# Kernel tuning notes

Measured on AMD Instinct MI355X. Metric: run time of the kernel, lower is better.

Reference implementation:

```python
import jax, jax.numpy as jnp
import numpy as np

B = 8192      # sessions
L = 64        # tokens per session
T = B * L     # total tokens
H = 128       # hidden_size
MAX_LEN = 64  # position_emb has MAX_LEN+1 rows


def setup_inputs() -> dict:
    key = jax.random.key(0)
    ks = jax.random.split(key, 10)
    s1 = 1.0 / np.sqrt(H)
    s2 = 1.0 / np.sqrt(2 * H)
    hidden = jax.random.normal(ks[0], (T, H), jnp.float32)
    seq_len = jnp.full((B,), L, dtype=jnp.int32)
    # reversed positions 1..L within each session (<= MAX_LEN)
    reverse_pos = jnp.tile(jnp.arange(L, 0, -1, dtype=jnp.int32), B)
    return {
        "hidden": hidden,
        "pos_table": jax.random.normal(ks[1], (MAX_LEN + 1, H), jnp.float32) * 0.02,
        "W_pos_w": jax.random.normal(ks[2], (H, 2 * H), jnp.float32) * s2,
        "W_pos_b": jax.random.normal(ks[3], (H,), jnp.float32) * s2,
        "W1_w": jax.random.normal(ks[4], (H, H), jnp.float32) * s1,
        "W1_b": jax.random.normal(ks[5], (H,), jnp.float32) * s1,
        "W2_w": jax.random.normal(ks[6], (H, H), jnp.float32) * s1,
        "W2_b": jax.random.normal(ks[7], (H,), jnp.float32) * s1,
        "q_w": jax.random.normal(ks[8], (1, H), jnp.float32) * s1,
        "q_b": jax.random.normal(ks[9], (1,), jnp.float32) * s1,
        "seq_len": seq_len,
        "reverse_pos": reverse_pos,
    }


def reference(hidden, pos_table, W_pos_w, W_pos_b, W1_w, W1_b, W2_w, W2_b,
              q_w, q_b, seq_len, reverse_pos):
    Bn = seq_len.shape[0]
    Tn = hidden.shape[0]
    # token -> session id (replaces the python split loop)
    seg = jnp.repeat(jnp.arange(Bn), seq_len, total_repeat_length=Tn)  # [T]
    # per-session mean, broadcast back to tokens (v_mean_repeat_concat)
    mean = jax.ops.segment_sum(hidden, seg, num_segments=Bn) \
        / seq_len[:, None].astype(hidden.dtype)                        # [B,H]
    mean_rep = mean[seg]                                               # [T,H]
    pos_emb = pos_table[reverse_pos]                                   # [T,H]
    pos_hidden = jnp.tanh(
        jnp.concatenate([hidden, pos_emb], axis=-1) @ W_pos_w.T + W_pos_b
    )                                                                  # [T,H]
    gate = jax.nn.sigmoid(mean_rep @ W1_w.T + W1_b + pos_hidden @ W2_w.T + W2_b)
    alpha = gate @ q_w.T + q_b                                         # [T,1]
    # per-session sum of alpha-weighted tokens (h_s)
    return jax.ops.segment_sum(alpha * hidden, seg, num_segments=Bn)   # [B,H]
```

## Files before the change

kernel.cpp:

```cpp
#include <hip/hip_runtime.h>
#include <hip/hip_bf16.h>

typedef unsigned short u16;
typedef __bf16 bf16x8 __attribute__((ext_vector_type(8)));
typedef float  f32x4  __attribute__((ext_vector_type(4)));

__device__ __forceinline__ unsigned pk2(float a, float b) {
    __hip_bfloat162 h = __float22bfloat162_rn(make_float2(a, b));
    unsigned u; __builtin_memcpy(&u, &h, 4);
    return u;
}
__device__ __forceinline__ u16 f2b1(float f) { return (u16)(pk2(f, f) & 0xFFFFu); }

#define MFMA __builtin_amdgcn_mfma_f32_16x16x32_bf16

__global__ __launch_bounds__(128) void prep_kernel(
    const float* __restrict__ pos_table, const float* __restrict__ Wpw,
    const float* __restrict__ Wpb, const float* __restrict__ W2,
    float* __restrict__ ppK, u16* __restrict__ wb1, u16* __restrict__ wb2)
{
    const int b = blockIdx.x, t = threadIdx.x;
    if (b < 65) {
        const float4* pr = (const float4*)(pos_table + b * 128);
        const float4* wr = (const float4*)(Wpw + t * 256 + 128);
        float acc = Wpb[t];
        #pragma unroll
        for (int k = 0; k < 32; ++k) {
            const float4 p = pr[k], wv = wr[k];
            acc += p.x * wv.x + p.y * wv.y + p.z * wv.z + p.w * wv.w;
        }
        ppK[b * 128 + t] = acc * 2.885390081777927f;
    } else {
        const int j = b - 65;
        const int off = (((j >> 4) * 4 + (t >> 5)) * 16 + (j & 15)) * 32 + (t & 31);
        wb1[off] = f2b1(Wpw[j * 256 + t]);
        wb2[off] = f2b1(W2[j * 128 + t]);
    }
}

__global__ __launch_bounds__(256, 4) void fused_kernel(
    const float* __restrict__ hidden, const int* __restrict__ rpos,
    const float* __restrict__ W1, const float* __restrict__ W1b,
    const float* __restrict__ W2b, const float* __restrict__ qw,
    const float* __restrict__ qb, const float* __restrict__ ppK,
    const u16* __restrict__ wb1g, const u16* __restrict__ wb2g,
    float* __restrict__ out)
{
    __shared__ __align__(16) u16 hbf[128 * 136];
    __shared__ float meanv[256];
    __shared__ float g1s[256];
    __shared__ float qws[128];
    __shared__ float alphas[128];
    __shared__ int   rps[128];

    const int tid = threadIdx.x;
    const int blk = blockIdx.x;
    const int w = tid >> 6;
    const int l = tid & 63;
    const int c = l & 15;
    const int g = l >> 4;
    const int R = 32 * w;
    const float* hsrc = hidden + (size_t)blk * (128 * 128);

    meanv[tid] = 0.f;
    if (tid < 128) { rps[tid] = rpos[blk * 128 + tid]; qws[tid] = qw[tid]; }
    __syncthreads();

    {
        float4 ms0 = {0.f, 0.f, 0.f, 0.f}, ms1 = {0.f, 0.f, 0.f, 0.f};
        #pragma unroll
        for (int i = 0; i < 16; ++i) {
            const int i4 = tid + i * 256;
            const float4 v = ((const float4*)hsrc)[i4];
            const int e = i4 * 4, row = e >> 7, col = e & 127;
            uint2 st; st.x = pk2(v.x, v.y); st.y = pk2(v.z, v.w);
            *(uint2*)&hbf[row * 136 + col] = st;
            if (i < 8) { ms0.x += v.x; ms0.y += v.y; ms0.z += v.z; ms0.w += v.w; }
            else       { ms1.x += v.x; ms1.y += v.y; ms1.z += v.z; ms1.w += v.w; }
        }
        ms0.x += __shfl_xor(ms0.x, 32, 64); ms0.y += __shfl_xor(ms0.y, 32, 64);
        ms0.z += __shfl_xor(ms0.z, 32, 64); ms0.w += __shfl_xor(ms0.w, 32, 64);
        ms1.x += __shfl_xor(ms1.x, 32, 64); ms1.y += __shfl_xor(ms1.y, 32, 64);
        ms1.z += __shfl_xor(ms1.z, 32, 64); ms1.w += __shfl_xor(ms1.w, 32, 64);
        if ((l & 32) == 0) {
            const int mc = (tid * 4) & 127;
            atomicAdd(&meanv[mc],           ms0.x); atomicAdd(&meanv[mc + 1],       ms0.y);
            atomicAdd(&meanv[mc + 2],       ms0.z); atomicAdd(&meanv[mc + 3],       ms0.w);
            atomicAdd(&meanv[128 + mc],     ms1.x); atomicAdd(&meanv[128 + mc + 1], ms1.y);
            atomicAdd(&meanv[128 + mc + 2], ms1.z); atomicAdd(&meanv[128 + mc + 3], ms1.w);
        }
    }
    __syncthreads();

    {
        const int col = tid & 127, s = tid >> 7;
        const float4* wr = (const float4*)(W1 + col * 128);
        const float4* mv = (const float4*)(meanv + s * 128);
        float acc = 0.f;
        #pragma unroll 8
        for (int k4 = 0; k4 < 32; ++k4) {
            const float4 wv = wr[k4], m4 = mv[k4];
            acc += m4.x * wv.x + m4.y * wv.y + m4.z * wv.z + m4.w * wv.w;
        }
        g1s[tid] = W1b[col] + W2b[col] + acc * (1.f / 64.f);
    }

    bf16x8 af[2][4];
    #pragma unroll
    for (int m = 0; m < 2; ++m)
        #pragma unroll
        for (int kk = 0; kk < 4; ++kk)
            af[m][kk] = *(const bf16x8*)&hbf[(R + 16 * m + c) * 136 + kk * 32 + g * 8];

    int pko[2][4];
    #pragma unroll
    for (int m = 0; m < 2; ++m)
        #pragma unroll
        for (int r = 0; r < 4; ++r)
            pko[m][r] = rps[R + 16 * m + 4 * g + r] * 128 + c;

    {
        const u16* wb1p = wb1g + c * 32 + g * 8;
        const float K2 = 2.885390081777927f;
        #pragma unroll
        for (int n = 0; n < 8; ++n) {
            f32x4 acc[2] = {};
            #pragma unroll
            for (int kk = 0; kk < 4; ++kk) {
                const bf16x8 bfr = *(const bf16x8*)(wb1p + n * 2048 + kk * 512);
                acc[0] = MFMA(af[0][kk], bfr, acc[0], 0, 0, 0);
                acc[1] = MFMA(af[1][kk], bfr, acc[1], 0, 0, 0);
            }
            #pragma unroll
            for (int m = 0; m < 2; ++m)
                #pragma unroll
                for (int r = 0; r < 4; ++r) {
                    const float arg = fmaf(acc[m][r], K2, ppK[pko[m][r] + 16 * n]);
                    const float e2 = __builtin_amdgcn_exp2f(arg);
                    const float rc = __builtin_amdgcn_rcpf(e2 + 1.f);
                    hbf[(R + 16 * m + 4 * g + r) * 136 + 16 * n + c] =
                        f2b1(fmaf(-2.f, rc, 1.f));
                }
        }
    }

    bf16x8 af2[2][4];
    #pragma unroll
    for (int m = 0; m < 2; ++m)
        #pragma unroll
        for (int kk = 0; kk < 4; ++kk)
            af2[m][kk] = *(const bf16x8*)&hbf[(R + 16 * m + c) * 136 + kk * 32 + g * 8];

    __syncthreads();

    {
        const u16* wb2p = wb2g + c * 32 + g * 8;
        const float K1 = 1.4426950408889634f;
        const int sw = w >> 1;
        float prt[2][4] = {};
        #pragma unroll
        for (int n = 0; n < 8; ++n) {
            f32x4 acc[2] = {};
            #pragma unroll
            for (int kk = 0; kk < 4; ++kk) {
                const bf16x8 bfr = *(const bf16x8*)(wb2p + n * 2048 + kk * 512);
                acc[0] = MFMA(af2[0][kk], bfr, acc[0], 0, 0, 0);
                acc[1] = MFMA(af2[1][kk], bfr, acc[1], 0, 0, 0);
            }
            const float gv = -K1 * g1s[sw * 128 + 16 * n + c];
            const float qv = qws[16 * n + c];
            #pragma unroll
            for (int m = 0; m < 2; ++m)
                #pragma unroll
                for (int r = 0; r < 4; ++r) {
                    const float arg = fmaf(acc[m][r], -K1, gv);
                    const float e2 = __builtin_amdgcn_exp2f(arg);
                    const float rc = __builtin_amdgcn_rcpf(e2 + 1.f);
                    prt[m][r] = fmaf(rc, qv, prt[m][r]);
                }
        }
        #pragma unroll
        for (int msk = 1; msk <= 8; msk <<= 1)
            #pragma unroll
            for (int m = 0; m < 2; ++m)
                #pragma unroll
                for (int r = 0; r < 4; ++r)
                    prt[m][r] += __shfl_xor(prt[m][r], msk, 64);
        if (c == 0) {
            const float qbv = qb[0];
            #pragma unroll
            for (int m = 0; m < 2; ++m)
                #pragma unroll
                for (int r = 0; r < 4; ++r)
                    alphas[R + 16 * m + 4 * g + r] = prt[m][r] + qbv;
        }
    }
    __syncthreads();

    {
        const int h = tid & 127, p = tid >> 7;
        const float* hs = hsrc + p * (64 * 128) + h;
        float accf = 0.f;
        #pragma unroll 8
        for (int t = 0; t < 64; ++t)
            accf = fmaf(alphas[64 * p + t], hs[t * 128], accf);
        out[(size_t)blk * 256 + tid] = accf;
    }
}

extern "C" void kernel_launch(void* const* d_in, const int* in_sizes, int n_in,
                              void* d_out, int out_size, void* d_ws, size_t ws_size,
                              hipStream_t stream)
{
    const float* hidden    = (const float*)d_in[0];
    const float* pos_table = (const float*)d_in[1];
    const float* Wpw       = (const float*)d_in[2];
    const float* Wpb       = (const float*)d_in[3];
    const float* W1w       = (const float*)d_in[4];
    const float* W1b       = (const float*)d_in[5];
    const float* W2w       = (const float*)d_in[6];
    const float* W2b       = (const float*)d_in[7];
    const float* qw        = (const float*)d_in[8];
    const float* qb        = (const float*)d_in[9];
    const int*   rpos      = (const int*)d_in[11];
    float* out = (float*)d_out;

    const int B = in_sizes[10];

    char* wsb = (char*)d_ws;
    float* ppK = (float*)wsb;
    u16* wb1   = (u16*)(wsb + 33280);
    u16* wb2   = (u16*)(wsb + 33280 + 32768);

    prep_kernel<<<193, 128, 0, stream>>>(pos_table, Wpw, Wpb, W2w,
                                         ppK, wb1, wb2);
    fused_kernel<<<B / 2, 256, 0, stream>>>(hidden, rpos, W1w, W1b, W2b, qw, qb,
                                            ppK, wb1, wb2, out);
}
```

Measured before the change: 481.4 us.

## Assign one session per wavefront and fold mean projection into MFMA

Restructures the fused kernel so each wavefront owns a whole 64-token session. The wavefront loads hidden straight from global into MFMA A-fragments and takes the session mean with shuffles instead of LDS atomics. The W1·mean product now runs as a bf16 MFMA seeded into the gate accumulator, using a W1 copy prepacked in the prep kernel, and the combined bias is precomputed there too. Most block-level barriers go away, but each wave now holds more registers (launch bounds drop to 2 waves/SIMD), and the mean projection loses some precision by moving to bf16.

```diff
diff --git a/kernel.cpp b/kernel.cpp
--- a/kernel.cpp
+++ b/kernel.cpp
@@ -12,12 +12,23 @@
 }
 __device__ __forceinline__ u16 f2b1(float f) { return (u16)(pk2(f, f) & 0xFFFFu); }
 
+__device__ __forceinline__ bf16x8 pack8(const float4 a, const float4 b) {
+    unsigned u0 = pk2(a.x, a.y), u1 = pk2(a.z, a.w);
+    unsigned u2 = pk2(b.x, b.y), u3 = pk2(b.z, b.w);
+    unsigned arr[4] = {u0, u1, u2, u3};
+    bf16x8 r; __builtin_memcpy(&r, arr, 16);
+    return r;
+}
+
 #define MFMA __builtin_amdgcn_mfma_f32_16x16x32_bf16
 
 __global__ __launch_bounds__(128) void prep_kernel(
     const float* __restrict__ pos_table, const float* __restrict__ Wpw,
     const float* __restrict__ Wpb, const float* __restrict__ W2,
-    float* __restrict__ ppK, u16* __restrict__ wb1, u16* __restrict__ wb2)
+    const float* __restrict__ W1, const float* __restrict__ W1b,
+    const float* __restrict__ W2b,
+    float* __restrict__ ppK, u16* __restrict__ wb1, u16* __restrict__ wb2,
+    u16* __restrict__ wb3, float* __restrict__ bsum)
 {
     const int b = blockIdx.x, t = threadIdx.x;
     if (b < 65) {
@@ -35,176 +46,188 @@
         const int off = (((j >> 4) * 4 + (t >> 5)) * 16 + (j & 15)) * 32 + (t & 31);
         wb1[off] = f2b1(Wpw[j * 256 + t]);
         wb2[off] = f2b1(W2[j * 128 + t]);
-    }
-}
-
-__global__ __launch_bounds__(256, 4) void fused_kernel(
+        wb3[off] = f2b1(W1[j * 128 + t]);
+        if (j == 0) bsum[t] = W1b[t] + W2b[t];
+    }
+}
+
+__global__ __launch_bounds__(256, 2) void fused_kernel(
     const float* __restrict__ hidden, const int* __restrict__ rpos,
-    const float* __restrict__ W1, const float* __restrict__ W1b,
-    const float* __restrict__ W2b, const float* __restrict__ qw,
-    const float* __restrict__ qb, const float* __restrict__ ppK,
-    const u16* __restrict__ wb1g, const u16* __restrict__ wb2g,
-    float* __restrict__ out)
+    const float* __restrict__ qw, const float* __restrict__ qb,
+    const float* __restrict__ ppK, const u16* __restrict__ wb1g,
+    const u16* __restrict__ wb2g, const u16* __restrict__ wb3g,
+    const float* __restrict__ bsum, float* __restrict__ out)
 {
-    __shared__ __align__(16) u16 hbf[128 * 136];
-    __shared__ float meanv[256];
-    __shared__ float g1s[256];
-    __shared__ float qws[128];
-    __shared__ float alphas[128];
-    __shared__ int   rps[128];
+    __shared__ __align__(16) u16 phs[4 * 64 * 136];
+    __shared__ __align__(16) float alphas[4 * 64];
 
     const int tid = threadIdx.x;
-    const int blk = blockIdx.x;
     const int w = tid >> 6;
     const int l = tid & 63;
     const int c = l & 15;
     const int g = l >> 4;
-    const int R = 32 * w;
-    const float* hsrc = hidden + (size_t)blk * (128 * 128);
-
-    meanv[tid] = 0.f;
-    if (tid < 128) { rps[tid] = rpos[blk * 128 + tid]; qws[tid] = qw[tid]; }
-    __syncthreads();
-
-    {
-        float4 ms0 = {0.f, 0.f, 0.f, 0.f}, ms1 = {0.f, 0.f, 0.f, 0.f};
-        #pragma unroll
-        for (int i = 0; i < 16; ++i) {
-            const int i4 = tid + i * 256;
-            const float4 v = ((const float4*)hsrc)[i4];
-            const int e = i4 * 4, row = e >> 7, col = e & 127;
-            uint2 st; st.x = pk2(v.x, v.y); st.y = pk2(v.z, v.w);
-            *(uint2*)&hbf[row * 136 + col] = st;
-            if (i < 8) { ms0.x += v.x; ms0.y += v.y; ms0.z += v.z; ms0.w += v.w; }
-            else       { ms1.x += v.x; ms1.y += v.y; ms1.z += v.z; ms1.w += v.w; }
-        }
-        ms0.x += __shfl_xor(ms0.x, 32, 64); ms0.y += __shfl_xor(ms0.y, 32, 64);
-        ms0.z += __shfl_xor(ms0.z, 32, 64); ms0.w += __shfl_xor(ms0.w, 32, 64);
-        ms1.x += __shfl_xor(ms1.x, 32, 64); ms1.y += __shfl_xor(ms1.y, 32, 64);
-        ms1.z += __shfl_xor(ms1.z, 32, 64); ms1.w += __shfl_xor(ms1.w, 32, 64);
-        if ((l & 32) == 0) {
-            const int mc = (tid * 4) & 127;
-            atomicAdd(&meanv[mc],           ms0.x); atomicAdd(&meanv[mc + 1],       ms0.y);
-            atomicAdd(&meanv[mc + 2],       ms0.z); atomicAdd(&meanv[mc + 3],       ms0.w);
-            atomicAdd(&meanv[128 + mc],     ms1.x); atomicAdd(&meanv[128 + mc + 1], ms1.y);
-            atomicAdd(&meanv[128 + mc + 2], ms1.z); atomicAdd(&meanv[128 + mc + 3], ms1.w);
-        }
-    }
-    __syncthreads();
-
-    {
-        const int col = tid & 127, s = tid >> 7;
-        const float4* wr = (const float4*)(W1 + col * 128);
-        const float4* mv = (const float4*)(meanv + s * 128);
-        float acc = 0.f;
-        #pragma unroll 8
-        for (int k4 = 0; k4 < 32; ++k4) {
-            const float4 wv = wr[k4], m4 = mv[k4];
-            acc += m4.x * wv.x + m4.y * wv.y + m4.z * wv.z + m4.w * wv.w;
-        }
-        g1s[tid] = W1b[col] + W2b[col] + acc * (1.f / 64.f);
-    }
-
-    bf16x8 af[2][4];
-    #pragma unroll
-    for (int m = 0; m < 2; ++m)
+    const int s = blockIdx.x * 4 + w;
+    const float* hs = hidden + (size_t)s * (64 * 128);
+    u16* ph = phs + w * (64 * 136);
+    float* alw = alphas + w * 64;
+
+    bf16x8 af[4][4];
+    float cs[4][8];
+    #pragma unroll
+    for (int kk = 0; kk < 4; ++kk)
+        #pragma unroll
+        for (int j = 0; j < 8; ++j) cs[kk][j] = 0.f;
+    #pragma unroll
+    for (int m = 0; m < 4; ++m)
+        #pragma unroll
+        for (int kk = 0; kk < 4; ++kk) {
+            const float4* p = (const float4*)(hs + (16 * m + c) * 128 + 32 * kk + 8 * g);
+            const float4 v0 = p[0], v1 = p[1];
+            cs[kk][0] += v0.x; cs[kk][1] += v0.y; cs[kk][2] += v0.z; cs[kk][3] += v0.w;
+            cs[kk][4] += v1.x; cs[kk][5] += v1.y; cs[kk][6] += v1.z; cs[kk][7] += v1.w;
+            af[m][kk] = pack8(v0, v1);
+        }
+
+    #pragma unroll
+    for (int msk = 1; msk <= 8; msk <<= 1)
         #pragma unroll
         for (int kk = 0; kk < 4; ++kk)
-            af[m][kk] = *(const bf16x8*)&hbf[(R + 16 * m + c) * 136 + kk * 32 + g * 8];
-
-    int pko[2][4];
-    #pragma unroll
-    for (int m = 0; m < 2; ++m)
-        #pragma unroll
-        for (int r = 0; r < 4; ++r)
-            pko[m][r] = rps[R + 16 * m + 4 * g + r] * 128 + c;
+            #pragma unroll
+            for (int j = 0; j < 8; ++j)
+                cs[kk][j] += __shfl_xor(cs[kk][j], msk, 64);
+    bf16x8 afm[4];
+    #pragma unroll
+    for (int kk = 0; kk < 4; ++kk) {
+        float4 a, b;
+        a.x = cs[kk][0] * (1.f / 64.f); a.y = cs[kk][1] * (1.f / 64.f);
+        a.z = cs[kk][2] * (1.f / 64.f); a.w = cs[kk][3] * (1.f / 64.f);
+        b.x = cs[kk][4] * (1.f / 64.f); b.y = cs[kk][5] * (1.f / 64.f);
+        b.z = cs[kk][6] * (1.f / 64.f); b.w = cs[kk][7] * (1.f / 64.f);
+        afm[kk] = pack8(a, b);
+    }
+
+    int pko[4][4];
+    {
+        const int* rp = rpos + s * 64;
+        #pragma unroll
+        for (int m = 0; m < 4; ++m) {
+            const int4 rv = *(const int4*)(rp + 16 * m + 4 * g);
+            pko[m][0] = rv.x * 128 + c; pko[m][1] = rv.y * 128 + c;
+            pko[m][2] = rv.z * 128 + c; pko[m][3] = rv.w * 128 + c;
+        }
+    }
 
     {
         const u16* wb1p = wb1g + c * 32 + g * 8;
         const float K2 = 2.885390081777927f;
         #pragma unroll
         for (int n = 0; n < 8; ++n) {
-            f32x4 acc[2] = {};
-            #pragma unroll
-            for (int kk = 0; kk < 4; ++kk) {
-                const bf16x8 bfr = *(const bf16x8*)(wb1p + n * 2048 + kk * 512);
-                acc[0] = MFMA(af[0][kk], bfr, acc[0], 0, 0, 0);
-                acc[1] = MFMA(af[1][kk], bfr, acc[1], 0, 0, 0);
+            float ppv[4][4];
+            #pragma unroll
+            for (int m = 0; m < 4; ++m)
+                #pragma unroll
+                for (int r = 0; r < 4; ++r)
+                    ppv[m][r] = ppK[pko[m][r] + 16 * n];
+            const bf16x8 b0 = *(const bf16x8*)(wb1p + n * 2048);
+            const bf16x8 b1 = *(const bf16x8*)(wb1p + n * 2048 + 512);
+            const bf16x8 b2 = *(const bf16x8*)(wb1p + n * 2048 + 1024);
+            const bf16x8 b3 = *(const bf16x8*)(wb1p + n * 2048 + 1536);
+            f32x4 acc[4] = {};
+            #pragma unroll
+            for (int m = 0; m < 4; ++m) {
+                acc[m] = MFMA(af[m][0], b0, acc[m], 0, 0, 0);
+                acc[m] = MFMA(af[m][1], b1, acc[m], 0, 0, 0);
+                acc[m] = MFMA(af[m][2], b2, acc[m], 0, 0, 0);
+                acc[m] = MFMA(af[m][3], b3, acc[m], 0, 0, 0);
             }
             #pragma unroll
-            for (int m = 0; m < 2; ++m)
+            for (int m = 0; m < 4; ++m)
                 #pragma unroll
                 for (int r = 0; r < 4; ++r) {
-                    const float arg = fmaf(acc[m][r], K2, ppK[pko[m][r] + 16 * n]);
+                    const float arg = fmaf(acc[m][r], K2, ppv[m][r]);
                     const float e2 = __builtin_amdgcn_exp2f(arg);
                     const float rc = __builtin_amdgcn_rcpf(e2 + 1.f);
-                    hbf[(R + 16 * m + 4 * g + r) * 136 + 16 * n + c] =
+                    ph[(16 * m + 4 * g + r) * 136 + 16 * n + c] =
                         f2b1(fmaf(-2.f, rc, 1.f));
                 }
         }
     }
 
-    bf16x8 af2[2][4];
-    #pragma unroll
-    for (int m = 0; m < 2; ++m)
+    bf16x8 af2[4][4];
+    #pragma unroll
+    for (int m = 0; m < 4; ++m)
         #pragma unroll
         for (int kk = 0; kk < 4; ++kk)
-            af2[m][kk] = *(const bf16x8*)&hbf[(R + 16 * m + c) * 136 + kk * 32 + g * 8];
-
-    __syncthreads();
+            af2[m][kk] = *(const bf16x8*)&ph[(16 * m + c) * 136 + kk * 32 + g * 8];
 
     {
         const u16* wb2p = wb2g + c * 32 + g * 8;
+        const u16* wb3p = wb3g + c * 32 + g * 8;
         const float K1 = 1.4426950408889634f;
-        const int sw = w >> 1;
-        float prt[2][4] = {};
+        float prt[4][4] = {};
         #pragma unroll
         for (int n = 0; n < 8; ++n) {
-            f32x4 acc[2] = {};
-            #pragma unroll
-            for (int kk = 0; kk < 4; ++kk) {
-                const bf16x8 bfr = *(const bf16x8*)(wb2p + n * 2048 + kk * 512);
-                acc[0] = MFMA(af2[0][kk], bfr, acc[0], 0, 0, 0);
-                acc[1] = MFMA(af2[1][kk], bfr, acc[1], 0, 0, 0);
-            }
-            const float gv = -K1 * g1s[sw * 128 + 16 * n + c];
-            const float qv = qws[16 * n + c];
-            #pragma unroll
-            for (int m = 0; m < 2; ++m)
+            const bf16x8 m0 = *(const bf16x8*)(wb3p + n * 2048);
+            const bf16x8 m1 = *(const bf16x8*)(wb3p + n * 2048 + 512);
+            const bf16x8 m2 = *(const bf16x8*)(wb3p + n * 2048 + 1024);
+            const bf16x8 m3 = *(const bf16x8*)(wb3p + n * 2048 + 1536);
+            f32x4 accM = {};
+            accM = MFMA(afm[0], m0, accM, 0, 0, 0);
+            accM = MFMA(afm[1], m1, accM, 0, 0, 0);
+            accM = MFMA(afm[2], m2, accM, 0, 0, 0);
+            accM = MFMA(afm[3], m3, accM, 0, 0, 0);
+            const bf16x8 b0 = *(const bf16x8*)(wb2p + n * 2048);
+            const bf16x8 b1 = *(const bf16x8*)(wb2p + n * 2048 + 512);
+            const bf16x8 b2 = *(const bf16x8*)(wb2p + n * 2048 + 1024);
+            const bf16x8 b3 = *(const bf16x8*)(wb2p + n * 2048 + 1536);
+            const float gvn = -K1 * bsum[16 * n + c];
+            const float qv  = qw[16 * n + c];
+            #pragma unroll
+            for (int m = 0; m < 4; ++m) {
+                f32x4 a = accM;
+                a = MFMA(af2[m][0], b0, a, 0, 0, 0);
+                a = MFMA(af2[m][1], b1, a, 0, 0, 0);
+                a = MFMA(af2[m][2], b2, a, 0, 0, 0);
+                a = MFMA(af2[m][3], b3, a, 0, 0, 0);
                 #pragma unroll
                 for (int r = 0; r < 4; ++r) {
-                    const float arg = fmaf(acc[m][r], -K1, gv);
+                    const float arg = fmaf(a[r], -K1, gvn);
                     const float e2 = __builtin_amdgcn_exp2f(arg);
                     const float rc = __builtin_amdgcn_rcpf(e2 + 1.f);
                     prt[m][r] = fmaf(rc, qv, prt[m][r]);
                 }
+            }
         }
         #pragma unroll
         for (int msk = 1; msk <= 8; msk <<= 1)
             #pragma unroll
-            for (int m = 0; m < 2; ++m)
+            for (int m = 0; m < 4; ++m)
                 #pragma unroll
                 for (int r = 0; r < 4; ++r)
                     prt[m][r] += __shfl_xor(prt[m][r], msk, 64);
         if (c == 0) {
             const float qbv = qb[0];
             #pragma unroll
-            for (int m = 0; m < 2; ++m)
+            for (int m = 0; m < 4; ++m)
                 #pragma unroll
                 for (int r = 0; r < 4; ++r)
-                    alphas[R + 16 * m + 4 * g + r] = prt[m][r] + qbv;
-        }
-    }
-    __syncthreads();
-
-    {
-        const int h = tid & 127, p = tid >> 7;
-        const float* hs = hsrc + p * (64 * 128) + h;
-        float accf = 0.f;
-        #pragma unroll 8
-        for (int t = 0; t < 64; ++t)
-            accf = fmaf(alphas[64 * p + t], hs[t * 128], accf);
-        out[(size_t)blk * 256 + tid] = accf;
+                    alw[16 * m + 4 * g + r] = prt[m][r] + qbv;
+        }
+    }
+
+    {
+        float a0[4] = {0.f, 0.f, 0.f, 0.f}, a1[4] = {0.f, 0.f, 0.f, 0.f};
+        #pragma unroll
+        for (int t4 = 0; t4 < 16; ++t4) {
+            const float4 av = *(const float4*)&alw[t4 * 4];
+            const float* hr = hs + (t4 * 4) * 128;
+            a0[0] = fmaf(av.x, hr[l], a0[0]);       a1[0] = fmaf(av.x, hr[64 + l], a1[0]);
+            a0[1] = fmaf(av.y, hr[128 + l], a0[1]); a1[1] = fmaf(av.y, hr[192 + l], a1[1]);
+            a0[2] = fmaf(av.z, hr[256 + l], a0[2]); a1[2] = fmaf(av.z, hr[320 + l], a1[2]);
+            a0[3] = fmaf(av.w, hr[384 + l], a0[3]); a1[3] = fmaf(av.w, hr[448 + l], a1[3]);
+        }
+        out[(size_t)s * 128 + l]      = (a0[0] + a0[1]) + (a0[2] + a0[3]);
+        out[(size_t)s * 128 + 64 + l] = (a1[0] + a1[1]) + (a1[2] + a1[3]);
     }
 }
 
@@ -228,12 +251,14 @@
     const int B = in_sizes[10];
 
     char* wsb = (char*)d_ws;
-    float* ppK = (float*)wsb;
-    u16* wb1   = (u16*)(wsb + 33280);
-    u16* wb2   = (u16*)(wsb + 33280 + 32768);
-
-    prep_kernel<<<193, 128, 0, stream>>>(pos_table, Wpw, Wpb, W2w,
-                                         ppK, wb1, wb2);
-    fused_kernel<<<B / 2, 256, 0, stream>>>(hidden, rpos, W1w, W1b, W2b, qw, qb,
-                                            ppK, wb1, wb2, out);
-}
+    float* ppK  = (float*)wsb;
+    u16*   wb1  = (u16*)(wsb + 33280);
+    u16*   wb2  = (u16*)(wsb + 33280 + 32768);
+    u16*   wb3  = (u16*)(wsb + 33280 + 2 * 32768);
+    float* bsum = (float*)(wsb + 33280 + 3 * 32768);
+
+    prep_kernel<<<193, 128, 0, stream>>>(pos_table, Wpw, Wpb, W2w, W1w, W1b, W2b,
+                                         ppK, wb1, wb2, wb3, bsum);
+    fused_kernel<<<B / 4, 256, 0, stream>>>(hidden, rpos, qw, qb,
+                                            ppK, wb1, wb2, wb3, bsum, out);
+}
```

Result: faster. 437.9 us (-9.0%).
